# Optimization experiments

Measured on AMD Instinct MI355X. Metric: run time of the kernel, lower is better.

The kernel has to match this reference:

```python
import jax, jax.numpy as jnp
import numpy as np

B, S, D, H, DFF = 8, 1024, 1024, 16, 4096
DK = D // H
EPS = 1e-6
NEG = -1e9


def _layer_norm(x, gamma, beta):
    # Faithful to hand-rolled LN: torch std is unbiased (ddof=1), eps added to sigma.
    mu = jnp.mean(x, axis=-1, keepdims=True)
    sigma = jnp.std(x, axis=-1, keepdims=True, ddof=1)
    return gamma * (x - mu) / (EPS + sigma) + beta


def setup_inputs() -> dict:
    key = jax.random.key(0)
    ks = jax.random.split(key, 12)
    s = 0.02
    inp = {
        "x": jax.random.normal(ks[0], (B, S, D), dtype=jnp.float32),
        "src_mask": jnp.ones((B, 1, 1, S), dtype=jnp.int32),
        "Wq": jax.random.normal(ks[1], (D, D), dtype=jnp.float32) * s,
        "bq": jnp.zeros((D,), dtype=jnp.float32),
        "Wk": jax.random.normal(ks[2], (D, D), dtype=jnp.float32) * s,
        "bk": jnp.zeros((D,), dtype=jnp.float32),
        "Wv": jax.random.normal(ks[3], (D, D), dtype=jnp.float32) * s,
        "bv": jnp.zeros((D,), dtype=jnp.float32),
        "Wo": jax.random.normal(ks[4], (D, D), dtype=jnp.float32) * s,
        "bo": jnp.zeros((D,), dtype=jnp.float32),
        "W1": jax.random.normal(ks[5], (DFF, D), dtype=jnp.float32) * s,
        "b1": jnp.zeros((DFF,), dtype=jnp.float32),
        "W2": jax.random.normal(ks[6], (D, DFF), dtype=jnp.float32) * s,
        "b2": jnp.zeros((D,), dtype=jnp.float32),
        "g1": jnp.ones((1,), dtype=jnp.float32),
        "be1": jnp.zeros((1,), dtype=jnp.float32),
        "g2": jnp.ones((1,), dtype=jnp.float32),
        "be2": jnp.zeros((1,), dtype=jnp.float32),
    }
    return inp


def _encoder_block(x, src_mask, Wq, bq, Wk, bk, Wv, bv, Wo, bo,
                   W1, b1, W2, b2, g1, be1, g2, be2):
    # Multi-head self-attention (dropout = identity in eval)
    def split(h):  # [B,S,D] -> [B,H,S,DK]
        return h.reshape(B, S, H, DK).transpose(0, 2, 1, 3)

    q = split(x @ Wq.T + bq)
    k = split(x @ Wk.T + bk)
    v = split(x @ Wv.T + bv)

    scores = jnp.einsum("bhqd,bhkd->bhqk", q, k) / jnp.sqrt(jnp.float32(DK))
    scores = jnp.where(src_mask == 0, NEG, scores)
    probs = jax.nn.softmax(scores, axis=-1)
    attn = jnp.einsum("bhqk,bhkd->bhqd", probs, v)
    attn = attn.transpose(0, 2, 1, 3).reshape(B, S, D)
    attn = attn @ Wo.T + bo

    x1 = _layer_norm(x + attn, g1, be1)

    ff = jax.nn.relu(x1 @ W1.T + b1) @ W2.T + b2
    x2 = _layer_norm(x1 + ff, g2, be2)
    return x2


def reference(x, src_mask, Wq, bq, Wk, bk, Wv, bv, Wo, bo,
              W1, b1, W2, b2, g1, be1, g2, be2):
    return _encoder_block(x, src_mask, Wq, bq, Wk, bk, Wv, bv, Wo, bo,
                          W1, b1, W2, b2, g1, be1, g2, be2)
```

## Files before the change

### kernel.cpp

```cpp
#include <hip/hip_runtime.h>
#include <stdint.h>

#define BB 8
#define SS 1024
#define DD 1024
#define HH 16
#define DFF 4096
#define MT (BB*SS)

typedef __attribute__((ext_vector_type(8))) short bf16x8;
typedef __attribute__((ext_vector_type(4))) short s16x4;
typedef __attribute__((ext_vector_type(4))) float f32x4;
typedef __attribute__((ext_vector_type(16))) float f32x16;
typedef unsigned int u32x2 __attribute__((ext_vector_type(2)));

#define LOG2E 1.44269504088896340736f

__device__ __forceinline__ short f2bf(float f) {
  union { float f; uint32_t u; } v; v.f = f;
  uint32_t r = v.u + 0x7FFFu + ((v.u >> 16) & 1u);
  return (short)(r >> 16);
}

__device__ __forceinline__ void gload_lds16(const void* g, void* l) {
  __builtin_amdgcn_global_load_lds(
      (__attribute__((address_space(1))) uint32_t*)(uintptr_t)g,
      (__attribute__((address_space(3))) uint32_t*)(uint32_t)(uintptr_t)l,
      16, 0, 0);
}

__device__ __forceinline__ uint32_t cvtpk(float lo, float hi) {
  uint32_t r;
  asm("v_cvt_pk_bf16_f32 %0, %1, %2" : "=v"(r) : "v"(lo), "v"(hi));
  return r;
}

__device__ __forceinline__ void swap2(uint32_t a, uint32_t b, uint32_t& x, uint32_t& y) {
#if __has_builtin(__builtin_amdgcn_permlane32_swap)
  u32x2 r = __builtin_amdgcn_permlane32_swap(a, b, false, false);
  x = r.x; y = r.y;
#else
  uint32_t asw = (uint32_t)__shfl_xor((int)a, 32, 64);
  uint32_t bsw = (uint32_t)__shfl_xor((int)b, 32, 64);
  bool h = (threadIdx.x & 32) != 0;
  x = h ? bsw : a;
  y = h ? b : asw;
#endif
}

__global__ __launch_bounds__(256) void cvt_bf16(const float* __restrict__ in,
                                                short* __restrict__ out, int n8) {
  int i = blockIdx.x * 256 + threadIdx.x;
  if (i >= n8) return;
  f32x4 a = *(const f32x4*)(in + (size_t)i * 8);
  f32x4 b = *(const f32x4*)(in + (size_t)i * 8 + 4);
  bf16x8 o;
  o[0]=f2bf(a[0]); o[1]=f2bf(a[1]); o[2]=f2bf(a[2]); o[3]=f2bf(a[3]);
  o[4]=f2bf(b[0]); o[5]=f2bf(b[1]); o[6]=f2bf(b[2]); o[7]=f2bf(b[3]);
  *(bf16x8*)(out + (size_t)i * 8) = o;
}

template<int BM, int RELU, int RES, int OUTF, int OUTB, int QKV>
__global__ __launch_bounds__(512, 2) void gemm_ring(
    const short* __restrict__ A, const short* __restrict__ W,
    const float* __restrict__ bq, const float* __restrict__ bk,
    const float* __restrict__ bv, const float* __restrict__ res,
    float* __restrict__ outF, short* __restrict__ outB,
    int M, int N, int K)
{
  constexpr int AISS   = BM / 128;
  constexpr int SLOT_A = BM * 32 * 2;
  constexpr int SLOT   = SLOT_A + 256 * 32 * 2;
  constexpr int MI     = BM / 32;
  __shared__ __align__(16) char lds[3 * SLOT];

  const int tid = threadIdx.x, lane = tid & 63, wid = tid >> 6;
  const int wm = wid >> 2, wn = wid & 3;
  const int lrow = lane & 15, lk = lane >> 4;

  const int nwg = gridDim.x;
  const int cpx = nwg >> 3;
  const int id  = blockIdx.x;
  const int wg  = (id & 7) * cpx + (id >> 3);
  const int gx  = N >> 8;
  const int bx  = wg % gx, by = wg / gx;
  const int row0 = by * BM, col0 = bx * 256;

  const int lineo = lane >> 3;
  const int rin   = lineo * 2 + ((lane >> 2) & 1);
  const int ksrc  = (lane & 3) ^ (lineo & 3);

  const short* Asrc[AISS];
#pragma unroll
  for (int j = 0; j < AISS; ++j)
    Asrc[j] = A + (size_t)(row0 + (wid * AISS + j) * 16 + rin) * K + ksrc * 8;
  const short* Bsrc[2];
#pragma unroll
  for (int j = 0; j < 2; ++j)
    Bsrc[j] = W + (size_t)(col0 + (wid * 2 + j) * 16 + rin) * K + ksrc * 8;

  const f32x4 z4 = {0.f, 0.f, 0.f, 0.f};
  f32x4 acc[MI][4];
#pragma unroll
  for (int i = 0; i < MI; ++i)
#pragma unroll
    for (int j = 0; j < 4; ++j) acc[i][j] = z4;

  const int NT = K >> 5;

  auto stage = [&](int ts, int s) {
    char* base = lds + s * SLOT;
    int ko = ts * 32;
#pragma unroll
    for (int j = 0; j < AISS; ++j)
      gload_lds16(Asrc[j] + ko, base + (wid * AISS + j) * 1024);
#pragma unroll
    for (int j = 0; j < 2; ++j)
      gload_lds16(Bsrc[j] + ko, base + SLOT_A + (wid * 2 + j) * 1024);
  };

  stage(0, 0);
  stage(1, 1);

  const int laneterm = (lrow >> 1) * 128 + (lrow & 1) * 64 + ((lk ^ ((lrow >> 1) & 3)) * 16);

  int sr = 0;
  for (int t = 0; t < NT; ++t) {
    const int sw = (sr == 0) ? 2 : sr - 1;
    const int ts = (t + 2 < NT) ? t + 2 : NT - 1;
    stage(ts, sw);
    if (AISS == 2) asm volatile("s_waitcnt vmcnt(8)" ::: "memory");
    else           asm volatile("s_waitcnt vmcnt(6)" ::: "memory");
    __builtin_amdgcn_s_barrier();
    __builtin_amdgcn_sched_barrier(0);

    const char* As = lds + sr * SLOT;
    const char* Bs = As + SLOT_A;
    bf16x8 af[MI], bfr[4];
#pragma unroll
    for (int mi = 0; mi < MI; ++mi)
      af[mi] = *(const bf16x8*)(As + wm * (BM * 32) + mi * 1024 + laneterm);
#pragma unroll
    for (int ni = 0; ni < 4; ++ni)
      bfr[ni] = *(const bf16x8*)(Bs + wn * 4096 + ni * 1024 + laneterm);

    __builtin_amdgcn_s_setprio(1);
#pragma unroll
    for (int mi = 0; mi < MI; ++mi)
#pragma unroll
      for (int ni = 0; ni < 4; ++ni)
        acc[mi][ni] = __builtin_amdgcn_mfma_f32_16x16x32_bf16(af[mi], bfr[ni], acc[mi][ni], 0, 0, 0);
    __builtin_amdgcn_s_setprio(0);

    __builtin_amdgcn_s_barrier();
    sr = (sr == 2) ? 0 : sr + 1;
  }

  const int sel    = QKV ? (col0 >> 10) : 0;
  const float* bias = QKV ? (sel == 0 ? bq : (sel == 1 ? bk : bv)) : bq;
  const int strideN = QKV ? 1024 : N;
  short* outBp = OUTB ? (outB + (QKV ? (size_t)sel * MT * DD : 0)) : outB;

#pragma unroll
  for (int mi = 0; mi < MI; ++mi) {
#pragma unroll
    for (int ni = 0; ni < 4; ++ni) {
      int col  = col0 + wn * 64 + ni * 16 + lrow;
      int coll = QKV ? (col & 1023) : col;
      float bvv = bias[coll];
#pragma unroll
      for (int r = 0; r < 4; ++r) {
        int row = row0 + wm * (BM / 2) + mi * 16 + lk * 4 + r;
        float v = acc[mi][ni][r] + bvv;
        if (RELU) v = fmaxf(v, 0.f);
        size_t idx = (size_t)row * strideN + coll;
        if (RES)  v += res[idx];
        if (OUTF) outF[idx] = v;
        if (OUTB) outBp[idx] = f2bf(v);
      }
    }
  }
}

__global__ __launch_bounds__(256) void transpose_v(const short* __restrict__ Vb,
                                                   short* __restrict__ Vt) {
  const int s = blockIdx.x * 256 + threadIdx.x;
  const int u = blockIdx.y;
  const int bh = blockIdx.z, b = bh >> 4, h = bh & 15;
  bf16x8 v = *(const bf16x8*)(Vb + ((size_t)(b * SS + s)) * DD + h * 64 + u * 8);
  size_t ob = ((size_t)bh * 64 + u * 8) * SS + s;
#pragma unroll
  for (int j = 0; j < 8; ++j) Vt[ob + (size_t)j * SS] = v[j];
}

__global__ __launch_bounds__(256) void attn_flash2(
    const short* __restrict__ Qm, const short* __restrict__ Km,
    const short* __restrict__ Vtg, const int* __restrict__ mask,
    short* __restrict__ Om)
{
  __shared__ short Ks[64 * 64];
  __shared__ short Vs[64 * 64];
  __shared__ float ma[64];
  __shared__ float fb[4 * 32];

  const int tid = threadIdx.x, lane = tid & 63, wid = tid >> 6;
  const int l31 = lane & 31, hi = lane >> 5;
  const int bh = blockIdx.y, b = bh >> 4, h = bh & 15;
  const int q0 = blockIdx.x * 128 + wid * 32;

  bf16x8 qf[4];
  {
    const short* qrow = Qm + ((size_t)(b * SS + q0 + l31)) * DD + h * 64;
#pragma unroll
    for (int t = 0; t < 4; ++t) qf[t] = *(const bf16x8*)(qrow + t * 16 + hi * 8);
  }

  f32x16 acc0, acc1;
#pragma unroll
  for (int i = 0; i < 16; ++i) { acc0[i] = 0.f; acc1[i] = 0.f; }
  float m_r = -3e38f, l_r = 0.f;

  const int srow = tid >> 3;
  const int su = tid & 7;

  for (int kt = 0; kt < SS; kt += 64) {
    __syncthreads();
#pragma unroll
    for (int i = 0; i < 2; ++i) {
      int r = i * 32 + srow;
      int uu = su ^ (r & 7);
      gload_lds16(Km + ((size_t)(b * SS + kt + r)) * DD + h * 64 + uu * 8,
                  Ks + i * 2048 + wid * 512);
      gload_lds16(Vtg + ((size_t)(bh * 64 + r)) * SS + kt + uu * 8,
                  Vs + i * 2048 + wid * 512);
    }
    if (tid < 64) ma[tid] = (mask[b * SS + kt + tid] == 0) ? -1e9f : 0.f;
    __syncthreads();

    f32x16 s0, s1;
#pragma unroll
    for (int i = 0; i < 16; ++i) { s0[i] = 0.f; s1[i] = 0.f; }
#pragma unroll
    for (int t = 0; t < 4; ++t) {
      int u = (t * 2 + hi) ^ (l31 & 7);
      bf16x8 k0 = *(const bf16x8*)(Ks + l31 * 64 + u * 8);
      bf16x8 k1 = *(const bf16x8*)(Ks + (32 + l31) * 64 + u * 8);
      s0 = __builtin_amdgcn_mfma_f32_32x32x16_bf16(k0, qf[t], s0, 0, 0, 0);
      s1 = __builtin_amdgcn_mfma_f32_32x32x16_bf16(k1, qf[t], s1, 0, 0, 0);
    }

    float p0[16], p1[16];
    float mx = -3e38f;
#pragma unroll
    for (int g = 0; g < 4; ++g) {
      f32x4 a0 = *(const f32x4*)(ma + g * 8 + hi * 4);
      f32x4 a1 = *(const f32x4*)(ma + 32 + g * 8 + hi * 4);
#pragma unroll
      for (int j = 0; j < 4; ++j) {
        float v0 = s0[g * 4 + j] * 0.125f + a0[j];
        float v1 = s1[g * 4 + j] * 0.125f + a1[j];
        p0[g * 4 + j] = v0; p1[g * 4 + j] = v1;
        mx = fmaxf(mx, fmaxf(v0, v1));
      }
    }
    mx = fmaxf(mx, __shfl_xor(mx, 32, 64));
    float mn  = fmaxf(m_r, mx);
    float fac = exp2f((m_r - mn) * LOG2E);
    m_r = mn;
    float mnl = mn * LOG2E;
    float rs = 0.f;
#pragma unroll
    for (int r = 0; r < 16; ++r) {
      p0[r] = exp2f(p0[r] * LOG2E - mnl);
      p1[r] = exp2f(p1[r] * LOG2E - mnl);
      rs += p0[r] + p1[r];
    }
    rs += __shfl_xor(rs, 32, 64);
    l_r = l_r * fac + rs;

    fb[wid * 32 + l31] = fac;
#pragma unroll
    for (int g = 0; g < 4; ++g) {
      f32x4 fv = *(const f32x4*)(fb + wid * 32 + g * 8 + hi * 4);
#pragma unroll
      for (int j = 0; j < 4; ++j) { acc0[g * 4 + j] *= fv[j]; acc1[g * 4 + j] *= fv[j]; }
    }

    uint32_t w0[8], w1[8];
#pragma unroll
    for (int m = 0; m < 8; ++m) {
      w0[m] = cvtpk(p0[2 * m], p0[2 * m + 1]);
      w1[m] = cvtpk(p1[2 * m], p1[2 * m + 1]);
    }
    uint32_t pa[4][4];
    swap2(w0[0], w0[2], pa[0][0], pa[0][2]);
    swap2(w0[1], w0[3], pa[0][1], pa[0][3]);
    swap2(w0[4], w0[6], pa[1][0], pa[1][2]);
    swap2(w0[5], w0[7], pa[1][1], pa[1][3]);
    swap2(w1[0], w1[2], pa[2][0], pa[2][2]);
    swap2(w1[1], w1[3], pa[2][1], pa[2][3]);
    swap2(w1[4], w1[6], pa[3][0], pa[3][2]);
    swap2(w1[5], w1[7], pa[3][1], pa[3][3]);

#pragma unroll
    for (int kc = 0; kc < 4; ++kc) {
      union { uint32_t w[4]; bf16x8 v; } pu;
      pu.w[0] = pa[kc][0]; pu.w[1] = pa[kc][1]; pu.w[2] = pa[kc][2]; pu.w[3] = pa[kc][3];
      int u = (kc * 2 + hi) ^ (l31 & 7);
      bf16x8 v0 = *(const bf16x8*)(Vs + l31 * 64 + u * 8);
      bf16x8 v1 = *(const bf16x8*)(Vs + (32 + l31) * 64 + u * 8);
      acc0 = __builtin_amdgcn_mfma_f32_32x32x16_bf16(pu.v, v0, acc0, 0, 0, 0);
      acc1 = __builtin_amdgcn_mfma_f32_32x32x16_bf16(pu.v, v1, acc1, 0, 0, 0);
    }
  }

  fb[wid * 32 + l31] = 1.f / l_r;
#pragma unroll
  for (int g = 0; g < 4; ++g) {
    f32x4 rv = *(const f32x4*)(fb + wid * 32 + g * 8 + hi * 4);
#pragma unroll
    for (int j = 0; j < 4; ++j) {
      int q = q0 + g * 8 + hi * 4 + j;
      size_t base = ((size_t)(b * SS + q)) * DD + h * 64 + l31;
      Om[base]      = f2bf(acc0[g * 4 + j] * rv[j]);
      Om[base + 32] = f2bf(acc1[g * 4 + j] * rv[j]);
    }
  }
}

template<int WRITE_BF16>
__global__ __launch_bounds__(256) void layernorm_k(
    float* __restrict__ x, short* __restrict__ xb,
    const float* __restrict__ g, const float* __restrict__ be)
{
  const int row = blockIdx.x, tid = threadIdx.x;
  float* xr = x + (size_t)row * DD;
  f32x4 a = *(const f32x4*)(xr + tid * 4);
  float s  = a[0] + a[1] + a[2] + a[3];
  float ss = a[0]*a[0] + a[1]*a[1] + a[2]*a[2] + a[3]*a[3];
#pragma unroll
  for (int o = 1; o < 64; o <<= 1) { s += __shfl_xor(s, o, 64); ss += __shfl_xor(ss, o, 64); }
  __shared__ float red[8];
  const int wid = tid >> 6, lane = tid & 63;
  if (lane == 0) { red[wid] = s; red[4 + wid] = ss; }
  __syncthreads();
  s  = red[0] + red[1] + red[2] + red[3];
  ss = red[4] + red[5] + red[6] + red[7];
  float mu  = s * (1.f / DD);
  float var = fmaxf((ss - (float)DD * mu * mu) * (1.f / (DD - 1)), 0.f);
  float inv = g[0] / (1e-6f + sqrtf(var));
  float bb  = be[0];
#pragma unroll
  for (int j = 0; j < 4; ++j) a[j] = (a[j] - mu) * inv + bb;
  *(f32x4*)(xr + tid * 4) = a;
  if (WRITE_BF16) {
    s16x4 o;
#pragma unroll
    for (int j = 0; j < 4; ++j) o[j] = f2bf(a[j]);
    *(s16x4*)(xb + (size_t)row * DD + tid * 4) = o;
  }
}

extern "C" void kernel_launch(void* const* d_in, const int* in_sizes, int n_in,
                              void* d_out, int out_size, void* d_ws, size_t ws_size,
                              hipStream_t stream) {
  const float* x    = (const float*)d_in[0];
  const int*   mask = (const int*)d_in[1];
  const float* Wq = (const float*)d_in[2];  const float* bq = (const float*)d_in[3];
  const float* Wk = (const float*)d_in[4];  const float* bk = (const float*)d_in[5];
  const float* Wv = (const float*)d_in[6];  const float* bv = (const float*)d_in[7];
  const float* Wo = (const float*)d_in[8];  const float* bo = (const float*)d_in[9];
  const float* W1 = (const float*)d_in[10]; const float* b1 = (const float*)d_in[11];
  const float* W2 = (const float*)d_in[12]; const float* b2 = (const float*)d_in[13];
  const float* g1 = (const float*)d_in[14]; const float* be1 = (const float*)d_in[15];
  const float* g2 = (const float*)d_in[16]; const float* be2 = (const float*)d_in[17];
  float* out = (float*)d_out;

  char* ws = (char*)d_ws;
  size_t off = 0;
  auto alloc = [&](size_t bytes) -> char* {
    char* p = ws + off; off += (bytes + 255) & ~(size_t)255; return p;
  };
  short* xb  = (short*)alloc((size_t)MT * DD * 2);
  short* wqb = (short*)alloc((size_t)DD * DD * 2);
  short* wkb = (short*)alloc((size_t)DD * DD * 2);
  short* wvb = (short*)alloc((size_t)DD * DD * 2);
  short* wob = (short*)alloc((size_t)DD * DD * 2);
  short* w1b = (short*)alloc((size_t)DFF * DD * 2);
  short* w2b = (short*)alloc((size_t)DD * DFF * 2);
  short* Qb  = (short*)alloc((size_t)MT * DD * 2);
  short* Kb  = (short*)alloc((size_t)MT * DD * 2);
  short* Vb  = (short*)alloc((size_t)MT * DD * 2);
  short* Ab  = (short*)alloc((size_t)MT * DD * 2);
  float* x1  = (float*)alloc((size_t)MT * DD * 4);
  short* F1  = Qb;
  short* x1b = xb;
  short* Vt  = (short*)x1;
  (void)wkb; (void)wvb; (void)Kb; (void)Vb;

  cvt_bf16<<<(MT * DD / 8 + 255) / 256, 256, 0, stream>>>(x, xb, MT * DD / 8);
  cvt_bf16<<<(DD * DD / 8 + 255) / 256, 256, 0, stream>>>(Wq, wqb, DD * DD / 8);
  cvt_bf16<<<(DD * DD / 8 + 255) / 256, 256, 0, stream>>>(Wk, wkb, DD * DD / 8);
  cvt_bf16<<<(DD * DD / 8 + 255) / 256, 256, 0, stream>>>(Wv, wvb, DD * DD / 8);
  cvt_bf16<<<(DD * DD / 8 + 255) / 256, 256, 0, stream>>>(Wo, wob, DD * DD / 8);
  cvt_bf16<<<(DFF * DD / 8 + 255) / 256, 256, 0, stream>>>(W1, w1b, DFF * DD / 8);
  cvt_bf16<<<(DD * DFF / 8 + 255) / 256, 256, 0, stream>>>(W2, w2b, DD * DFF / 8);

  gemm_ring<256,0,0,0,1,1><<<dim3((3072/256)*(MT/256)), 512, 0, stream>>>(
      xb, wqb, bq, bk, bv, nullptr, nullptr, Qb, MT, 3072, DD);

  transpose_v<<<dim3(SS/256, 8, BB*HH), 256, 0, stream>>>(Vb, Vt);
  attn_flash2<<<dim3(SS/128, BB*HH), 256, 0, stream>>>(Qb, Kb, Vt, mask, Ab);

  gemm_ring<128,0,1,1,0,0><<<dim3((DD/256)*(MT/128)), 512, 0, stream>>>(
      Ab, wob, bo, bo, bo, x, x1, nullptr, MT, DD, DD);
  layernorm_k<1><<<MT, 256, 0, stream>>>(x1, x1b, g1, be1);

  gemm_ring<256,1,0,0,1,0><<<dim3((DFF/256)*(MT/256)), 512, 0, stream>>>(
      x1b, w1b, b1, b1, b1, nullptr, nullptr, F1, MT, DFF, DD);
  gemm_ring<128,0,1,1,0,0><<<dim3((DD/256)*(MT/128)), 512, 0, stream>>>(
      F1, w2b, b2, b2, b2, x1, out, nullptr, MT, DD, DFF);
  layernorm_k<0><<<MT, 256, 0, stream>>>(out, nullptr, g2, be2);
}
```

Measured before the change: 400.8 us.

## Double-buffer attention K/V tiles, fold softmax scale into Q, add lazy rescale

The attention kernel now double-buffers K and V tiles in LDS, issuing the next tile's loads before computing on the current one, and loads the whole mask row once up front. The 1/sqrt(dk)*log2e scale is folded into the Q projection epilogue, which removes per-element multiplies in the softmax. Rescaling of the running max is skipped unless the new max exceeds the old one by more than 8 in the log2 domain. The QKV and FFN1 GEMMs also move from 256-row to 128-row tiles. The cost is more LDS per block, a slight precision change because Q is scaled before rounding to bf16, and unnormalized exponentials up to 2^8 inside a tile.

```diff
diff --git a/kernel.cpp b/kernel.cpp
--- a/kernel.cpp
+++ b/kernel.cpp
@@ -66,7 +66,7 @@
     const float* __restrict__ bq, const float* __restrict__ bk,
     const float* __restrict__ bv, const float* __restrict__ res,
     float* __restrict__ outF, short* __restrict__ outB,
-    int M, int N, int K)
+    int M, int N, int K, float qscale)
 {
   constexpr int AISS   = BM / 128;
   constexpr int SLOT_A = BM * 32 * 2;
@@ -160,6 +160,7 @@
   const float* bias = QKV ? (sel == 0 ? bq : (sel == 1 ? bk : bv)) : bq;
   const int strideN = QKV ? 1024 : N;
   short* outBp = OUTB ? (outB + (QKV ? (size_t)sel * MT * DD : 0)) : outB;
+  const float scl = (QKV && sel == 0) ? qscale : 1.f;
 
 #pragma unroll
   for (int mi = 0; mi < MI; ++mi) {
@@ -172,6 +173,7 @@
       for (int r = 0; r < 4; ++r) {
         int row = row0 + wm * (BM / 2) + mi * 16 + lk * 4 + r;
         float v = acc[mi][ni][r] + bvv;
+        if (QKV) v *= scl;
         if (RELU) v = fmaxf(v, 0.f);
         size_t idx = (size_t)row * strideN + coll;
         if (RES)  v += res[idx];
@@ -193,14 +195,14 @@
   for (int j = 0; j < 8; ++j) Vt[ob + (size_t)j * SS] = v[j];
 }
 
-__global__ __launch_bounds__(256) void attn_flash2(
+__global__ __launch_bounds__(256) void attn_flash3(
     const short* __restrict__ Qm, const short* __restrict__ Km,
     const short* __restrict__ Vtg, const int* __restrict__ mask,
     short* __restrict__ Om)
 {
-  __shared__ short Ks[64 * 64];
-  __shared__ short Vs[64 * 64];
-  __shared__ float ma[64];
+  __shared__ short KsB[2 * 64 * 64];
+  __shared__ short VsB[2 * 64 * 64];
+  __shared__ float ma_all[SS];
   __shared__ float fb[4 * 32];
 
   const int tid = threadIdx.x, lane = tid & 63, wid = tid >> 6;
@@ -208,6 +210,15 @@
   const int bh = blockIdx.y, b = bh >> 4, h = bh & 15;
   const int q0 = blockIdx.x * 128 + wid * 32;
 
+  {
+    const int* mrow = mask + b * SS;
+#pragma unroll
+    for (int i = 0; i < 4; ++i) {
+      int idx = i * 256 + tid;
+      ma_all[idx] = (mrow[idx] == 0) ? -1.442695e9f : 0.f;
+    }
+  }
+
   bf16x8 qf[4];
   {
     const short* qrow = Qm + ((size_t)(b * SS + q0 + l31)) * DD + h * 64;
@@ -223,68 +234,86 @@
   const int srow = tid >> 3;
   const int su = tid & 7;
 
-  for (int kt = 0; kt < SS; kt += 64) {
-    __syncthreads();
+  auto stageKV = [&](int kt2, int bi) {
 #pragma unroll
     for (int i = 0; i < 2; ++i) {
       int r = i * 32 + srow;
       int uu = su ^ (r & 7);
-      gload_lds16(Km + ((size_t)(b * SS + kt + r)) * DD + h * 64 + uu * 8,
-                  Ks + i * 2048 + wid * 512);
-      gload_lds16(Vtg + ((size_t)(bh * 64 + r)) * SS + kt + uu * 8,
-                  Vs + i * 2048 + wid * 512);
-    }
-    if (tid < 64) ma[tid] = (mask[b * SS + kt + tid] == 0) ? -1e9f : 0.f;
-    __syncthreads();
+      gload_lds16(Km + ((size_t)(b * SS + kt2 + r)) * DD + h * 64 + uu * 8,
+                  KsB + bi * 4096 + (i * 256 + wid * 64) * 8);
+      gload_lds16(Vtg + ((size_t)(bh * 64 + r)) * SS + kt2 + uu * 8,
+                  VsB + bi * 4096 + (i * 256 + wid * 64) * 8);
+    }
+  };
+
+  __syncthreads();
+  stageKV(0, 0);
+
+  for (int t = 0; t < 16; ++t) {
+    if (t < 15) {
+      stageKV((t + 1) << 6, (t + 1) & 1);
+      asm volatile("s_waitcnt vmcnt(4)" ::: "memory");
+    } else {
+      asm volatile("s_waitcnt vmcnt(0)" ::: "memory");
+    }
+    __builtin_amdgcn_s_barrier();
+    __builtin_amdgcn_sched_barrier(0);
+
+    const short* Ks = KsB + (t & 1) * 4096;
+    const short* Vs = VsB + (t & 1) * 4096;
 
     f32x16 s0, s1;
 #pragma unroll
     for (int i = 0; i < 16; ++i) { s0[i] = 0.f; s1[i] = 0.f; }
 #pragma unroll
-    for (int t = 0; t < 4; ++t) {
-      int u = (t * 2 + hi) ^ (l31 & 7);
+    for (int t4 = 0; t4 < 4; ++t4) {
+      int u = (t4 * 2 + hi) ^ (l31 & 7);
       bf16x8 k0 = *(const bf16x8*)(Ks + l31 * 64 + u * 8);
       bf16x8 k1 = *(const bf16x8*)(Ks + (32 + l31) * 64 + u * 8);
-      s0 = __builtin_amdgcn_mfma_f32_32x32x16_bf16(k0, qf[t], s0, 0, 0, 0);
-      s1 = __builtin_amdgcn_mfma_f32_32x32x16_bf16(k1, qf[t], s1, 0, 0, 0);
-    }
-
+      s0 = __builtin_amdgcn_mfma_f32_32x32x16_bf16(k0, qf[t4], s0, 0, 0, 0);
+      s1 = __builtin_amdgcn_mfma_f32_32x32x16_bf16(k1, qf[t4], s1, 0, 0, 0);
+    }
+
+    const float* map = ma_all + (t << 6);
     float p0[16], p1[16];
     float mx = -3e38f;
 #pragma unroll
     for (int g = 0; g < 4; ++g) {
-      f32x4 a0 = *(const f32x4*)(ma + g * 8 + hi * 4);
-      f32x4 a1 = *(const f32x4*)(ma + 32 + g * 8 + hi * 4);
+      f32x4 a0 = *(const f32x4*)(map + g * 8 + hi * 4);
+      f32x4 a1 = *(const f32x4*)(map + 32 + g * 8 + hi * 4);
 #pragma unroll
       for (int j = 0; j < 4; ++j) {
-        float v0 = s0[g * 4 + j] * 0.125f + a0[j];
-        float v1 = s1[g * 4 + j] * 0.125f + a1[j];
+        float v0 = s0[g * 4 + j] + a0[j];
+        float v1 = s1[g * 4 + j] + a1[j];
         p0[g * 4 + j] = v0; p1[g * 4 + j] = v1;
         mx = fmaxf(mx, fmaxf(v0, v1));
       }
     }
     mx = fmaxf(mx, __shfl_xor(mx, 32, 64));
-    float mn  = fmaxf(m_r, mx);
-    float fac = exp2f((m_r - mn) * LOG2E);
-    m_r = mn;
-    float mnl = mn * LOG2E;
+
+    if (!__all(mx <= m_r + 8.f)) {
+      float mn  = fmaxf(m_r, mx);
+      float fac = exp2f(m_r - mn);
+      m_r = mn;
+      l_r *= fac;
+      fb[wid * 32 + l31] = fac;
+#pragma unroll
+      for (int g = 0; g < 4; ++g) {
+        f32x4 fv = *(const f32x4*)(fb + wid * 32 + g * 8 + hi * 4);
+#pragma unroll
+        for (int j = 0; j < 4; ++j) { acc0[g * 4 + j] *= fv[j]; acc1[g * 4 + j] *= fv[j]; }
+      }
+    }
+
     float rs = 0.f;
 #pragma unroll
     for (int r = 0; r < 16; ++r) {
-      p0[r] = exp2f(p0[r] * LOG2E - mnl);
-      p1[r] = exp2f(p1[r] * LOG2E - mnl);
+      p0[r] = exp2f(p0[r] - m_r);
+      p1[r] = exp2f(p1[r] - m_r);
       rs += p0[r] + p1[r];
     }
     rs += __shfl_xor(rs, 32, 64);
-    l_r = l_r * fac + rs;
-
-    fb[wid * 32 + l31] = fac;
-#pragma unroll
-    for (int g = 0; g < 4; ++g) {
-      f32x4 fv = *(const f32x4*)(fb + wid * 32 + g * 8 + hi * 4);
-#pragma unroll
-      for (int j = 0; j < 4; ++j) { acc0[g * 4 + j] *= fv[j]; acc1[g * 4 + j] *= fv[j]; }
-    }
+    l_r += rs;
 
     uint32_t w0[8], w1[8];
 #pragma unroll
@@ -312,6 +341,8 @@
       acc0 = __builtin_amdgcn_mfma_f32_32x32x16_bf16(pu.v, v0, acc0, 0, 0, 0);
       acc1 = __builtin_amdgcn_mfma_f32_32x32x16_bf16(pu.v, v1, acc1, 0, 0, 0);
     }
+
+    __builtin_amdgcn_s_barrier();
   }
 
   fb[wid * 32 + l31] = 1.f / l_r;
@@ -398,6 +429,8 @@
   short* Vt  = (short*)x1;
   (void)wkb; (void)wvb; (void)Kb; (void)Vb;
 
+  const float qscale = 0.125f * LOG2E;
+
   cvt_bf16<<<(MT * DD / 8 + 255) / 256, 256, 0, stream>>>(x, xb, MT * DD / 8);
   cvt_bf16<<<(DD * DD / 8 + 255) / 256, 256, 0, stream>>>(Wq, wqb, DD * DD / 8);
   cvt_bf16<<<(DD * DD / 8 + 255) / 256, 256, 0, stream>>>(Wk, wkb, DD * DD / 8);
@@ -406,19 +439,19 @@
   cvt_bf16<<<(DFF * DD / 8 + 255) / 256, 256, 0, stream>>>(W1, w1b, DFF * DD / 8);
   cvt_bf16<<<(DD * DFF / 8 + 255) / 256, 256, 0, stream>>>(W2, w2b, DD * DFF / 8);
 
-  gemm_ring<256,0,0,0,1,1><<<dim3((3072/256)*(MT/256)), 512, 0, stream>>>(
-      xb, wqb, bq, bk, bv, nullptr, nullptr, Qb, MT, 3072, DD);
+  gemm_ring<128,0,0,0,1,1><<<dim3((3072/256)*(MT/128)), 512, 0, stream>>>(
+      xb, wqb, bq, bk, bv, nullptr, nullptr, Qb, MT, 3072, DD, qscale);
 
   transpose_v<<<dim3(SS/256, 8, BB*HH), 256, 0, stream>>>(Vb, Vt);
-  attn_flash2<<<dim3(SS/128, BB*HH), 256, 0, stream>>>(Qb, Kb, Vt, mask, Ab);
+  attn_flash3<<<dim3(SS/128, BB*HH), 256, 0, stream>>>(Qb, Kb, Vt, mask, Ab);
 
   gemm_ring<128,0,1,1,0,0><<<dim3((DD/256)*(MT/128)), 512, 0, stream>>>(
-      Ab, wob, bo, bo, bo, x, x1, nullptr, MT, DD, DD);
+      Ab, wob, bo, bo, bo, x, x1, nullptr, MT, DD, DD, 1.f);
   layernorm_k<1><<<MT, 256, 0, stream>>>(x1, x1b, g1, be1);
 
-  gemm_ring<256,1,0,0,1,0><<<dim3((DFF/256)*(MT/256)), 512, 0, stream>>>(
-      x1b, w1b, b1, b1, b1, nullptr, nullptr, F1, MT, DFF, DD);
+  gemm_ring<128,1,0,0,1,0><<<dim3((DFF/256)*(MT/128)), 512, 0, stream>>>(
+      x1b, w1b, b1, b1, b1, nullptr, nullptr, F1, MT, DFF, DD, 1.f);
   gemm_ring<128,0,1,1,0,0><<<dim3((DD/256)*(MT/128)), 512, 0, stream>>>(
-      F1, w2b, b2, b2, b2, x1, out, nullptr, MT, DD, DFF);
+      F1, w2b, b2, b2, b2, x1, out, nullptr, MT, DD, DFF, 1.f);
   layernorm_k<0><<<MT, 256, 0, stream>>>(out, nullptr, g2, be2);
 }
```

Result: faster. 386.0 us (-3.7%).
